# Optimization experiments

Measured on AMD Instinct MI355X. Metric: run time of the kernel, lower is better.

The kernel has to match this reference:

```python
import jax, jax.numpy as jnp
import numpy as np

B, N, H, L = 4096, 512, 1024, 8


def setup_inputs() -> dict:
    key = jax.random.key(0)
    k1, k2, k3, k4 = jax.random.split(key, 4)
    x = jax.random.normal(k1, (B, N), dtype=jnp.float32)
    beta = jax.random.uniform(k2, (H, L, N), dtype=jnp.float32)  # torch.rand init
    bound = 1.0 / np.sqrt(N)
    W = jax.random.uniform(k3, (H, N), minval=-bound, maxval=bound, dtype=jnp.float32)
    b = jax.random.uniform(k4, (H,), minval=-bound, maxval=bound, dtype=jnp.float32)
    return {"x": x, "beta": beta, "W": W, "b": b}


def reference(x, beta, W, b):
    # Original computes c[h,j,k] = sum_l beta[h,l,j]*beta[h,l,k], then
    # out_fm[b,h] = sum_{j<k} x[b,j]*x[b,k]*c[h,j,k]  (strict upper-tri mask).
    # FM identity: sum_{j<k} x_j x_k <v_j, v_k>
    #            = 0.5 * sum_l [ (sum_j x_j v_{lj})^2 - sum_j x_j^2 v_{lj}^2 ]
    s = jnp.einsum('bn,hln->bhl', x, beta)            # (B, H, L)
    ssq = jnp.einsum('bn,hln->bhl', x * x, beta * beta)  # (B, H, L)
    fm = 0.5 * jnp.sum(s * s - ssq, axis=-1)          # (B, H)
    linear_out = x @ W.T + b                          # (B, H)
    return fm + linear_out
```

## Files before the change

### kernel.cpp

```cpp
#include <hip/hip_runtime.h>
#include <stdint.h>

static constexpr int B_DIM = 4096;
static constexpr int N_DIM = 512;
static constexpr int H_DIM = 1024;
static constexpr int L_DIM = 8;
static constexpr int HL    = H_DIM * L_DIM;
static constexpr int KC    = 2 * N_DIM;

typedef __attribute__((ext_vector_type(8))) short short8;
typedef __attribute__((ext_vector_type(8))) unsigned short u16x8;
typedef __attribute__((ext_vector_type(4))) float f32x4;

__device__ __forceinline__ uint16_t f2bf(float f) {
  uint32_t u = __float_as_uint(f);
  u += 0x7fffu + ((u >> 16) & 1u);
  return (uint16_t)(u >> 16);
}

__device__ __forceinline__ void stage16(const uint16_t* g, uint16_t* l) {
  __builtin_amdgcn_global_load_lds(
      (const __attribute__((address_space(1))) void*)g,
      (__attribute__((address_space(3))) void*)l, 16, 0, 0);
}

static constexpr int PREP_T0 = HL * N_DIM / 8;
static constexpr int PREP_T1 = B_DIM * N_DIM / 8;
static constexpr int PREP_T2 = H_DIM * N_DIM / 8;

__global__ void prep_kernel(const float* __restrict__ x, const float* __restrict__ beta,
                            const float* __restrict__ W,
                            uint16_t* __restrict__ xcomb, uint16_t* __restrict__ betab,
                            uint16_t* __restrict__ combW) {
  int t = blockIdx.x * 256 + threadIdx.x;
  if (t < PREP_T0) {
    const f32x4* src = (const f32x4*)(beta + (size_t)t * 8);
    f32x4 a = src[0], b = src[1];
    u16x8 o;
#pragma unroll
    for (int i = 0; i < 4; ++i) { o[i] = f2bf(a[i]); o[4 + i] = f2bf(b[i]); }
    *(u16x8*)(betab + (size_t)t * 8) = o;
    return;
  }
  t -= PREP_T0;
  if (t < PREP_T1) {
    int bb = t >> 6, n8 = (t & 63) * 8;
    const f32x4* src = (const f32x4*)(x + (size_t)bb * N_DIM + n8);
    f32x4 a = src[0], b = src[1];
    u16x8 lo, hi;
#pragma unroll
    for (int i = 0; i < 4; ++i) {
      lo[i] = f2bf(a[i]);        lo[4 + i] = f2bf(b[i]);
      hi[i] = f2bf(a[i] * a[i]); hi[4 + i] = f2bf(b[i] * b[i]);
    }
    *(u16x8*)(xcomb + (size_t)bb * KC + n8)         = lo;
    *(u16x8*)(xcomb + (size_t)bb * KC + N_DIM + n8) = hi;
    return;
  }
  t -= PREP_T1;
  int h = t >> 6, n8 = (t & 63) * 8;
  const f32x4* wsrc = (const f32x4*)(W + (size_t)h * N_DIM + n8);
  f32x4 wa = wsrc[0], wb = wsrc[1];
  u16x8 lo;
#pragma unroll
  for (int i = 0; i < 4; ++i) { lo[i] = f2bf(wa[i]); lo[4 + i] = f2bf(wb[i]); }
  *(u16x8*)(combW + (size_t)h * KC + n8) = lo;
  float s[8] = {};
#pragma unroll
  for (int l = 0; l < L_DIM; ++l) {
    const f32x4* bsrc = (const f32x4*)(beta + ((size_t)h * L_DIM + l) * N_DIM + n8);
    f32x4 a = bsrc[0], b = bsrc[1];
#pragma unroll
    for (int i = 0; i < 4; ++i) { s[i] += a[i] * a[i]; s[4 + i] += b[i] * b[i]; }
  }
  u16x8 hi;
#pragma unroll
  for (int i = 0; i < 8; ++i) hi[i] = f2bf(-0.5f * s[i]);
  *(u16x8*)(combW + (size_t)h * KC + N_DIM + n8) = hi;
}

static constexpr int S_BUF  = 13312;
static constexpr int OFF_A2 = 4096;
static constexpr int OFF_B  = 8192;
static constexpr int OFF_W  = 12288;

template<bool ODD>
__device__ __forceinline__ void compute_tile(
    const uint16_t* __restrict__ L,
    const int (&offA)[4], const int (&offB)[4], int offW,
    f32x4 (&acc)[4][4], f32x4 (&lacc)[4])
{
  short8 bf[4];
#pragma unroll
  for (int j = 0; j < 4; ++j) bf[j] = *(const short8*)(L + offB[j]);
  short8 wf = *(const short8*)(L + offW);
  __builtin_amdgcn_s_setprio(1);
#pragma unroll
  for (int i = 0; i < 4; ++i) {
    short8 a = *(const short8*)(L + offA[i]);
    short8 a2;
    if constexpr (ODD) a2 = *(const short8*)(L + OFF_A2 + offA[i]);
    else               a2 = a;
#pragma unroll
    for (int j = 0; j < 4; ++j)
      acc[i][j] = __builtin_amdgcn_mfma_f32_16x16x32_bf16(a, bf[j], acc[i][j], 0, 0, 0);
    lacc[i] = __builtin_amdgcn_mfma_f32_16x16x32_bf16(a2, wf, lacc[i], 0, 0, 0);
  }
  __builtin_amdgcn_s_setprio(0);
}

__global__ __launch_bounds__(256) void fm_kernel(
    const uint16_t* __restrict__ xcomb,
    const uint16_t* __restrict__ betab,
    const uint16_t* __restrict__ combW,
    const float* __restrict__ bias,
    float* __restrict__ out)
{
  __shared__ __align__(16) uint16_t lds[3 * S_BUF];

  const int tid  = threadIdx.x;
  const int lane = tid & 63;
  const int wave = tid >> 6;
  const int wm = wave >> 1, wn = wave & 1;
  const int fr = lane & 15, quad = lane >> 4;

  const int bid = blockIdx.x;
  const int cid = (bid & 7) * 256 + (bid >> 3);
  const int bx = cid >> 5, by = cid & 31;
  const int row0 = by * 128, col0 = bx * 128, hcol0 = bx * 16;

  const int s0 = tid, s1 = tid + 256;
  const int m0 = s0 >> 2, c0 = (s0 & 3) ^ ((m0 + (m0 >> 2)) & 3);
  const int m1 = s1 >> 2, c1 = (s1 & 3) ^ ((m1 + (m1 >> 2)) & 3);
  const uint16_t* baseA0 = xcomb + (size_t)(row0 + m0) * KC + c0 * 8;
  const uint16_t* baseA1 = xcomb + (size_t)(row0 + m1) * KC + c1 * 8;
  const uint16_t* baseB0 = betab + (size_t)(col0 + m0) * N_DIM + c0 * 8;
  const uint16_t* baseB1 = betab + (size_t)(col0 + m1) * N_DIM + c1 * 8;
  const int d0 = s0 * 8, d1 = s1 * 8;
  const int sW = tid & 127;
  const int mW = sW >> 3, cpW = sW & 7, cW = cpW ^ (mW & 7);
  const uint16_t* baseW = combW + (size_t)(hcol0 + mW) * KC
                        + (cW < 4 ? cW * 8 : N_DIM + (cW - 4) * 8);
  const int dW = sW * 8;

  int offA[4], offB[4], offW_;
#pragma unroll
  for (int i = 0; i < 4; ++i) {
    int m = wm * 64 + i * 16 + fr;
    offA[i] = (m * 4 + (quad ^ ((m + (m >> 2)) & 3))) * 8;
  }
#pragma unroll
  for (int j = 0; j < 4; ++j) {
    int m = wn * 64 + j * 16 + fr;
    offB[j] = OFF_B + (m * 4 + (quad ^ ((m + (m >> 2)) & 3))) * 8;
  }
  offW_ = OFF_W + (fr * 8 + ((wn * 4 + quad) ^ (fr & 7))) * 8;

  f32x4 acc[4][4] = {};
  f32x4 lacc[4]   = {};

  auto STAGE = [&](uint16_t* Lp, int kt) {
    stage16(baseA0 + kt, Lp + d0);
    stage16(baseA1 + kt, Lp + d1);
    stage16(baseA0 + N_DIM + kt, Lp + OFF_A2 + d0);
    stage16(baseA1 + N_DIM + kt, Lp + OFF_A2 + d1);
    stage16(baseB0 + kt, Lp + OFF_B + d0);
    stage16(baseB1 + kt, Lp + OFF_B + d1);
    stage16(baseW + kt, Lp + OFF_W + dW);
  };

  STAGE(lds, 0);
  STAGE(lds + S_BUF, 32);
  asm volatile("s_waitcnt vmcnt(7)" ::: "memory");
  __builtin_amdgcn_s_barrier();

  int bc = 0;
  for (int t = 0; t < 14; ++t) {
    int b2 = bc + 2; if (b2 >= 3) b2 -= 3;
    STAGE(lds + b2 * S_BUF, (t + 2) * 32);
    const uint16_t* L = lds + bc * S_BUF;
    if (wn) compute_tile<true >(L, offA, offB, offW_, acc, lacc);
    else    compute_tile<false>(L, offA, offB, offW_, acc, lacc);
    asm volatile("s_waitcnt vmcnt(7)" ::: "memory");
    __builtin_amdgcn_s_barrier();
    bc = (bc == 2) ? 0 : bc + 1;
  }
  {
    const uint16_t* L = lds + 2 * S_BUF;
    if (wn) compute_tile<true >(L, offA, offB, offW_, acc, lacc);
    else    compute_tile<false>(L, offA, offB, offW_, acc, lacc);
    asm volatile("s_waitcnt vmcnt(0)" ::: "memory");
    __builtin_amdgcn_s_barrier();
  }
  {
    const uint16_t* L = lds;
    if (wn) compute_tile<true >(L, offA, offB, offW_, acc, lacc);
    else    compute_tile<false>(L, offA, offB, offW_, acc, lacc);
  }
  __syncthreads();

  float* red = (float*)lds;
  if (!wn) {
#pragma unroll
    for (int i = 0; i < 4; ++i)
#pragma unroll
      for (int r = 0; r < 4; ++r)
        red[(wm * 64 + i * 16 + quad * 4 + r) * 20 + fr] = lacc[i][r];
  }
  __syncthreads();
  if (wn) {
#pragma unroll
    for (int i = 0; i < 4; ++i)
#pragma unroll
      for (int r = 0; r < 4; ++r)
        red[(wm * 64 + i * 16 + quad * 4 + r) * 20 + fr] += lacc[i][r];
  }
  __syncthreads();
#pragma unroll
  for (int i = 0; i < 4; ++i)
#pragma unroll
    for (int j = 0; j < 4; ++j) {
      const int hin = wn * 8 + j * 2 + (fr >> 3);
#pragma unroll
      for (int r = 0; r < 4; ++r) {
        float v = acc[i][j][r];
        v = v * v;
        v += __shfl_xor(v, 1);
        v += __shfl_xor(v, 2);
        v += __shfl_xor(v, 4);
        if ((lane & 7) == 0)
          red[(wm * 64 + i * 16 + quad * 4 + r) * 20 + hin] += 0.5f * v;
      }
    }
  __syncthreads();
  {
    const int row = tid >> 1, hb = (tid & 1) * 8;
    const float* rp = red + row * 20 + hb;
    const float* bp = bias + hcol0 + hb;
    float* op = out + (size_t)(row0 + row) * H_DIM + hcol0 + hb;
    f32x4 v0 = *(const f32x4*)(rp);
    f32x4 v1 = *(const f32x4*)(rp + 4);
    f32x4 b0 = *(const f32x4*)(bp);
    f32x4 b1 = *(const f32x4*)(bp + 4);
    *(f32x4*)(op)     = v0 + b0;
    *(f32x4*)(op + 4) = v1 + b1;
  }
}

extern "C" void kernel_launch(void* const* d_in, const int* in_sizes, int n_in,
                              void* d_out, int out_size, void* d_ws, size_t ws_size,
                              hipStream_t stream) {
  const float* x    = (const float*)d_in[0];
  const float* beta = (const float*)d_in[1];
  const float* W    = (const float*)d_in[2];
  const float* bias = (const float*)d_in[3];
  float* out = (float*)d_out;

  uint16_t* xcomb = (uint16_t*)d_ws;
  uint16_t* betab = xcomb + (size_t)B_DIM * KC;
  uint16_t* combW = betab + (size_t)HL * N_DIM;

  const int prep_threads = PREP_T0 + PREP_T1 + PREP_T2;
  prep_kernel<<<prep_threads / 256, 256, 0, stream>>>(x, beta, W, xcomb, betab, combW);

  fm_kernel<<<2048, 256, 0, stream>>>(xcomb, betab, combW, bias, out);
}
```

Baseline: 186.2 us.

## Compute x squared in registers and switch to double-buffered LDS pipeline

The prep kernel no longer writes a bf16 x-squared copy. Odd waves now square the bf16 x fragment in registers before the linear/ssq MFMA, which removes the x² half of the A staging traffic and its global writes and reads. The LDS pipeline also drops from three buffers with partial vmcnt waits to two buffers with full __syncthreads. This cuts LDS use and global traffic, but adds VALU work per tile. It squares an already-rounded bf16 x, which adds a little rounding error, and the simpler sync may expose more load latency.

```diff
diff --git a/kernel.cpp b/kernel.cpp
--- a/kernel.cpp
+++ b/kernel.cpp
@@ -11,6 +11,7 @@
 typedef __attribute__((ext_vector_type(8))) short short8;
 typedef __attribute__((ext_vector_type(8))) unsigned short u16x8;
 typedef __attribute__((ext_vector_type(4))) float f32x4;
+typedef __attribute__((ext_vector_type(4))) unsigned int u32x4;
 
 __device__ __forceinline__ uint16_t f2bf(float f) {
   uint32_t u = __float_as_uint(f);
@@ -24,13 +25,27 @@
       (__attribute__((address_space(3))) void*)l, 16, 0, 0);
 }
 
+__device__ __forceinline__ short8 sq8(short8 a) {
+  u32x4 r;
+#pragma unroll
+  for (int p = 0; p < 4; ++p) {
+    float f0 = __uint_as_float(((uint32_t)(uint16_t)a[2 * p])     << 16);
+    float f1 = __uint_as_float(((uint32_t)(uint16_t)a[2 * p + 1]) << 16);
+    float s0 = f0 * f0, s1 = f1 * f1;
+    uint32_t pk;
+    asm("v_cvt_pk_bf16_f32 %0, %1, %2" : "=v"(pk) : "v"(s0), "v"(s1));
+    r[p] = pk;
+  }
+  return __builtin_bit_cast(short8, r);
+}
+
 static constexpr int PREP_T0 = HL * N_DIM / 8;
 static constexpr int PREP_T1 = B_DIM * N_DIM / 8;
 static constexpr int PREP_T2 = H_DIM * N_DIM / 8;
 
 __global__ void prep_kernel(const float* __restrict__ x, const float* __restrict__ beta,
                             const float* __restrict__ W,
-                            uint16_t* __restrict__ xcomb, uint16_t* __restrict__ betab,
+                            uint16_t* __restrict__ xonly, uint16_t* __restrict__ betab,
                             uint16_t* __restrict__ combW) {
   int t = blockIdx.x * 256 + threadIdx.x;
   if (t < PREP_T0) {
@@ -47,14 +62,10 @@
     int bb = t >> 6, n8 = (t & 63) * 8;
     const f32x4* src = (const f32x4*)(x + (size_t)bb * N_DIM + n8);
     f32x4 a = src[0], b = src[1];
-    u16x8 lo, hi;
-#pragma unroll
-    for (int i = 0; i < 4; ++i) {
-      lo[i] = f2bf(a[i]);        lo[4 + i] = f2bf(b[i]);
-      hi[i] = f2bf(a[i] * a[i]); hi[4 + i] = f2bf(b[i] * b[i]);
-    }
-    *(u16x8*)(xcomb + (size_t)bb * KC + n8)         = lo;
-    *(u16x8*)(xcomb + (size_t)bb * KC + N_DIM + n8) = hi;
+    u16x8 lo;
+#pragma unroll
+    for (int i = 0; i < 4; ++i) { lo[i] = f2bf(a[i]); lo[4 + i] = f2bf(b[i]); }
+    *(u16x8*)(xonly + (size_t)bb * N_DIM + n8) = lo;
     return;
   }
   t -= PREP_T1;
@@ -79,10 +90,9 @@
   *(u16x8*)(combW + (size_t)h * KC + N_DIM + n8) = hi;
 }
 
-static constexpr int S_BUF  = 13312;
-static constexpr int OFF_A2 = 4096;
-static constexpr int OFF_B  = 8192;
-static constexpr int OFF_W  = 12288;
+static constexpr int S_BUF = 9216;
+static constexpr int OFF_B = 4096;
+static constexpr int OFF_W = 8192;
 
 template<bool ODD>
 __device__ __forceinline__ void compute_tile(
@@ -98,25 +108,25 @@
 #pragma unroll
   for (int i = 0; i < 4; ++i) {
     short8 a = *(const short8*)(L + offA[i]);
-    short8 a2;
-    if constexpr (ODD) a2 = *(const short8*)(L + OFF_A2 + offA[i]);
-    else               a2 = a;
 #pragma unroll
     for (int j = 0; j < 4; ++j)
       acc[i][j] = __builtin_amdgcn_mfma_f32_16x16x32_bf16(a, bf[j], acc[i][j], 0, 0, 0);
-    lacc[i] = __builtin_amdgcn_mfma_f32_16x16x32_bf16(a2, wf, lacc[i], 0, 0, 0);
+    short8 al;
+    if constexpr (ODD) al = sq8(a);
+    else               al = a;
+    lacc[i] = __builtin_amdgcn_mfma_f32_16x16x32_bf16(al, wf, lacc[i], 0, 0, 0);
   }
   __builtin_amdgcn_s_setprio(0);
 }
 
 __global__ __launch_bounds__(256) void fm_kernel(
-    const uint16_t* __restrict__ xcomb,
+    const uint16_t* __restrict__ xonly,
     const uint16_t* __restrict__ betab,
     const uint16_t* __restrict__ combW,
     const float* __restrict__ bias,
     float* __restrict__ out)
 {
-  __shared__ __align__(16) uint16_t lds[3 * S_BUF];
+  __shared__ __align__(16) uint16_t lds[2 * S_BUF];
 
   const int tid  = threadIdx.x;
   const int lane = tid & 63;
@@ -132,16 +142,16 @@
   const int s0 = tid, s1 = tid + 256;
   const int m0 = s0 >> 2, c0 = (s0 & 3) ^ ((m0 + (m0 >> 2)) & 3);
   const int m1 = s1 >> 2, c1 = (s1 & 3) ^ ((m1 + (m1 >> 2)) & 3);
-  const uint16_t* baseA0 = xcomb + (size_t)(row0 + m0) * KC + c0 * 8;
-  const uint16_t* baseA1 = xcomb + (size_t)(row0 + m1) * KC + c1 * 8;
+  const uint16_t* baseA0 = xonly + (size_t)(row0 + m0) * N_DIM + c0 * 8;
+  const uint16_t* baseA1 = xonly + (size_t)(row0 + m1) * N_DIM + c1 * 8;
   const uint16_t* baseB0 = betab + (size_t)(col0 + m0) * N_DIM + c0 * 8;
   const uint16_t* baseB1 = betab + (size_t)(col0 + m1) * N_DIM + c1 * 8;
-  const int d0 = s0 * 8, d1 = s1 * 8;
+  const int d0 = s0 * 8;
   const int sW = tid & 127;
   const int mW = sW >> 3, cpW = sW & 7, cW = cpW ^ (mW & 7);
   const uint16_t* baseW = combW + (size_t)(hcol0 + mW) * KC
                         + (cW < 4 ? cW * 8 : N_DIM + (cW - 4) * 8);
-  const int dW = sW * 8;
+  const int dW = OFF_W + sW * 8;
 
   int offA[4], offB[4], offW_;
 #pragma unroll
@@ -161,41 +171,27 @@
 
   auto STAGE = [&](uint16_t* Lp, int kt) {
     stage16(baseA0 + kt, Lp + d0);
-    stage16(baseA1 + kt, Lp + d1);
-    stage16(baseA0 + N_DIM + kt, Lp + OFF_A2 + d0);
-    stage16(baseA1 + N_DIM + kt, Lp + OFF_A2 + d1);
+    stage16(baseA1 + kt, Lp + d0 + 2048);
     stage16(baseB0 + kt, Lp + OFF_B + d0);
-    stage16(baseB1 + kt, Lp + OFF_B + d1);
-    stage16(baseW + kt, Lp + OFF_W + dW);
+    stage16(baseB1 + kt, Lp + OFF_B + d0 + 2048);
+    stage16(baseW + kt, Lp + dW);
   };
 
   STAGE(lds, 0);
-  STAGE(lds + S_BUF, 32);
-  asm volatile("s_waitcnt vmcnt(7)" ::: "memory");
-  __builtin_amdgcn_s_barrier();
-
-  int bc = 0;
-  for (int t = 0; t < 14; ++t) {
-    int b2 = bc + 2; if (b2 >= 3) b2 -= 3;
-    STAGE(lds + b2 * S_BUF, (t + 2) * 32);
-    const uint16_t* L = lds + bc * S_BUF;
-    if (wn) compute_tile<true >(L, offA, offB, offW_, acc, lacc);
-    else    compute_tile<false>(L, offA, offB, offW_, acc, lacc);
-    asm volatile("s_waitcnt vmcnt(7)" ::: "memory");
-    __builtin_amdgcn_s_barrier();
-    bc = (bc == 2) ? 0 : bc + 1;
+  __syncthreads();
+
+  for (int t = 0; t < 15; ++t) {
+    uint16_t* nxt       = lds + ((t & 1) ^ 1) * S_BUF;
+    const uint16_t* cur = lds + (t & 1) * S_BUF;
+    STAGE(nxt, (t + 1) * 32);
+    if (wn) compute_tile<true >(cur, offA, offB, offW_, acc, lacc);
+    else    compute_tile<false>(cur, offA, offB, offW_, acc, lacc);
+    __syncthreads();
   }
   {
-    const uint16_t* L = lds + 2 * S_BUF;
-    if (wn) compute_tile<true >(L, offA, offB, offW_, acc, lacc);
-    else    compute_tile<false>(L, offA, offB, offW_, acc, lacc);
-    asm volatile("s_waitcnt vmcnt(0)" ::: "memory");
-    __builtin_amdgcn_s_barrier();
-  }
-  {
-    const uint16_t* L = lds;
-    if (wn) compute_tile<true >(L, offA, offB, offW_, acc, lacc);
-    else    compute_tile<false>(L, offA, offB, offW_, acc, lacc);
+    const uint16_t* cur = lds + S_BUF;
+    if (wn) compute_tile<true >(cur, offA, offB, offW_, acc, lacc);
+    else    compute_tile<false>(cur, offA, offB, offW_, acc, lacc);
   }
   __syncthreads();
 
@@ -256,12 +252,12 @@
   const float* bias = (const float*)d_in[3];
   float* out = (float*)d_out;
 
-  uint16_t* xcomb = (uint16_t*)d_ws;
-  uint16_t* betab = xcomb + (size_t)B_DIM * KC;
+  uint16_t* xonly = (uint16_t*)d_ws;
+  uint16_t* betab = xonly + (size_t)B_DIM * N_DIM;
   uint16_t* combW = betab + (size_t)HL * N_DIM;
 
   const int prep_threads = PREP_T0 + PREP_T1 + PREP_T2;
-  prep_kernel<<<prep_threads / 256, 256, 0, stream>>>(x, beta, W, xcomb, betab, combW);
-
-  fm_kernel<<<2048, 256, 0, stream>>>(xcomb, betab, combW, bias, out);
-}
+  prep_kernel<<<prep_threads / 256, 256, 0, stream>>>(x, beta, W, xonly, betab, combW);
+
+  fm_kernel<<<2048, 256, 0, stream>>>(xonly, betab, combW, bias, out);
+}
```

Result: faster. 172.9 us (-7.1%).
